# Performance work log

Hardware: AMD Instinct MI355X
Metric: run time of the kernel (lower is better)

Reference implementation:

```python
import jax, jax.numpy as jnp
import numpy as np

N_NODES = 50000
N_EDGES = 800000
N_GRAPHS = 2500
IN_DIM = 128
HID = 64
HEADS = 2
NEG_SLOPE = 0.2


def _gat_layer(x, W, att_src, att_dst, bias, src, dst, n):
    # W: [F_in, H*C], att_*: [H, C], bias: [C]
    h = (x @ W).reshape(n, HEADS, HID)            # [N,H,C]
    a_src = jnp.sum(h * att_src[None], axis=-1)   # [N,H]
    a_dst = jnp.sum(h * att_dst[None], axis=-1)   # [N,H]
    e = jax.nn.leaky_relu(a_src[src] + a_dst[dst], NEG_SLOPE)  # [E,H]
    # segment softmax over destination neighborhoods
    m = jax.ops.segment_max(e, dst, num_segments=n)            # [N,H]
    m = jnp.where(jnp.isfinite(m), m, 0.0)
    ex = jnp.exp(e - m[dst])
    s = jax.ops.segment_sum(ex, dst, num_segments=n)           # [N,H]
    alpha = ex / jnp.maximum(s[dst], 1e-16)                    # [E,H]
    msg = h[src] * alpha[:, :, None]                           # [E,H,C]
    out = jax.ops.segment_sum(msg, dst, num_segments=n)        # [N,H,C]
    return out.mean(axis=1) + bias                             # concat=False -> head mean


def _with_self_loops(edge_index, n):
    loop = jnp.arange(n, dtype=edge_index.dtype)
    src = jnp.concatenate([edge_index[0], loop])
    dst = jnp.concatenate([edge_index[1], loop])
    return src, dst


def setup_inputs() -> dict:
    key = jax.random.key(0)
    ks = jax.random.split(key, 16)
    x = jax.random.normal(ks[0], (N_NODES, IN_DIM), dtype=jnp.float32)
    edge_index = jax.random.randint(ks[1], (2, N_EDGES), 0, N_NODES, dtype=jnp.int32)
    batch = jnp.sort(jax.random.randint(ks[2], (N_NODES,), 0, N_GRAPHS, dtype=jnp.int32))

    def glorot(k, shape):
        fan = shape[0] + shape[-1]
        return jax.random.normal(k, shape, dtype=jnp.float32) * np.sqrt(2.0 / fan)

    inp = {"x": x, "edge_index": edge_index, "batch": batch}
    dims = [IN_DIM, HID, HID]
    for i in range(3):
        inp[f"W{i+1}"] = glorot(ks[3 + 4 * i], (dims[i], HEADS * HID))
        inp[f"att_src{i+1}"] = glorot(ks[4 + 4 * i], (HEADS, HID))
        inp[f"att_dst{i+1}"] = glorot(ks[5 + 4 * i], (HEADS, HID))
        inp[f"b{i+1}"] = jnp.zeros((HID,), dtype=jnp.float32)
    inp["lin_w"] = glorot(ks[15], (HID, 1))
    inp["lin_b"] = jnp.zeros((1,), dtype=jnp.float32)
    return inp


def reference(x, W1, att_src1, att_dst1, b1, W2, att_src2, att_dst2, b2,
              W3, att_src3, att_dst3, b3, lin_w, lin_b, edge_index, batch):
    n = x.shape[0]
    src, dst = _with_self_loops(edge_index, n)
    h = jax.nn.relu(_gat_layer(x, W1, att_src1, att_dst1, b1, src, dst, n))
    h = jax.nn.relu(_gat_layer(h, W2, att_src2, att_dst2, b2, src, dst, n))
    h = jax.nn.relu(_gat_layer(h, W3, att_src3, att_dst3, b3, src, dst, n))
    # global mean pool over graphs
    sums = jax.ops.segment_sum(h, batch, num_segments=N_GRAPHS)          # [G,C]
    cnt = jax.ops.segment_sum(jnp.ones((n,), h.dtype), batch, num_segments=N_GRAPHS)
    pooled = sums / jnp.maximum(cnt, 1.0)[:, None]
    return pooled @ lin_w + lin_b                                        # [G,1]
```

## Files before the change

### kernel.cpp

```cpp
#include <hip/hip_runtime.h>
#include <hip/hip_fp16.h>
#include <math.h>


__device__ __forceinline__ float lrelu(float v) { return v > 0.f ? v : 0.2f * v; }

__device__ __forceinline__ float wave_max(float v) {
  for (int off = 32; off; off >>= 1) v = fmaxf(v, __shfl_xor(v, off, 64));
  return v;
}
__device__ __forceinline__ float half_sum(float v) {
  for (int off = 16; off; off >>= 1) v += __shfl_xor(v, off, 64);
  return v;
}
__device__ __forceinline__ float half_max(float v) {
  for (int off = 16; off; off >>= 1) v = fmaxf(v, __shfl_xor(v, off, 64));
  return v;
}

__global__ void count_rank(const int* __restrict__ ei, int* __restrict__ deg,
                           int* __restrict__ rank, int e) {
  int j0 = blockIdx.x * 1024 + threadIdx.x;
#pragma unroll
  for (int k = 0; k < 4; ++k) {
    int j = j0 + k * 256;
    if (j < e) rank[j] = atomicAdd(&deg[ei[e + j]], 1);
  }
}

__global__ void scan_blocks(const int* __restrict__ deg, int* __restrict__ row_ptr,
                            int* __restrict__ btot, int n) {
  __shared__ int sm[256];
  int i = blockIdx.x * 256 + threadIdx.x;
  int v = (i < n) ? deg[i] : 0;
  sm[threadIdx.x] = v;
  __syncthreads();
  for (int off = 1; off < 256; off <<= 1) {
    int t = (threadIdx.x >= off) ? sm[threadIdx.x - off] : 0;
    __syncthreads();
    sm[threadIdx.x] += t;
    __syncthreads();
  }
  if (i < n) row_ptr[i] = sm[threadIdx.x] - v;
  if (threadIdx.x == 255) btot[blockIdx.x] = sm[255];
}

__global__ void scan_totals(int* __restrict__ btot, int nb) {
  __shared__ int sm[256];
  int v = (threadIdx.x < nb) ? btot[threadIdx.x] : 0;
  sm[threadIdx.x] = v;
  __syncthreads();
  for (int off = 1; off < 256; off <<= 1) {
    int t = (threadIdx.x >= off) ? sm[threadIdx.x - off] : 0;
    __syncthreads();
    sm[threadIdx.x] += t;
    __syncthreads();
  }
  if (threadIdx.x < nb) btot[threadIdx.x] = sm[threadIdx.x] - v;
}

__global__ void scan_add(int* __restrict__ row_ptr, int* __restrict__ csr,
                         const int* __restrict__ btot, int n, int total) {
  int i = blockIdx.x * 256 + threadIdx.x;
  if (i < n) {
    int v = row_ptr[i] + btot[blockIdx.x] + i;
    row_ptr[i] = v;
    csr[v] = i;
  }
  if (i == 0) row_ptr[n] = total;
}

__global__ void place_kernel(const int* __restrict__ ei, const int* __restrict__ rank,
                             const int* __restrict__ row_ptr, int* __restrict__ csr,
                             int e) {
  int j0 = blockIdx.x * 1024 + threadIdx.x;
#pragma unroll
  for (int k = 0; k < 4; ++k) {
    int j = j0 + k * 256;
    if (j < e) {
      int d = ei[e + j];
      csr[row_ptr[d] + 1 + rank[j]] = ei[j];
    }
  }
}

template <int K>
__global__ __launch_bounds__(256) void gemm_att(const float* __restrict__ X,
                                                const float* __restrict__ W,
                                                const float* __restrict__ asw,
                                                const float* __restrict__ adw,
                                                __half* __restrict__ H16,
                                                float* __restrict__ a_src,
                                                float* __restrict__ a_dst, int N) {
  __shared__ float Xs[64 * (K + 4)];
  int tid = threadIdx.x;
  int row0 = blockIdx.x * 64;
  int head = blockIdx.y;

  for (int idx = tid; idx < 64 * K; idx += 256) {
    int r = idx / K;
    int k = idx - r * K;
    int gr = row0 + r;
    if (gr >= N) gr = N - 1;
    Xs[r * (K + 4) + k] = X[(size_t)gr * K + k];
  }
  __syncthreads();

  int cgrp = tid & 15;
  int rg = tid >> 4;
  int c0 = head * 64 + cgrp * 4;
  const float* wp = W + c0;
  float acc[4][4] = {};

#pragma unroll 2
  for (int k = 0; k < K; k += 4) {
    float4 xr[4];
#pragma unroll
    for (int j = 0; j < 4; ++j)
      xr[j] = *(const float4*)(&Xs[(rg * 4 + j) * (K + 4) + k]);
#pragma unroll
    for (int kk = 0; kk < 4; ++kk) {
      float4 w4 = *(const float4*)(wp + (k + kk) * 128);
#pragma unroll
      for (int j = 0; j < 4; ++j) {
        float xv = ((const float*)&xr[j])[kk];
        acc[j][0] = fmaf(xv, w4.x, acc[j][0]);
        acc[j][1] = fmaf(xv, w4.y, acc[j][1]);
        acc[j][2] = fmaf(xv, w4.z, acc[j][2]);
        acc[j][3] = fmaf(xv, w4.w, acc[j][3]);
      }
    }
  }

  float4 aw = *(const float4*)(asw + c0);
  float4 dw = *(const float4*)(adw + c0);
#pragma unroll
  for (int j = 0; j < 4; ++j) {
    int r = row0 + rg * 4 + j;
    float sp = acc[j][0] * aw.x + acc[j][1] * aw.y + acc[j][2] * aw.z + acc[j][3] * aw.w;
    float dp = acc[j][0] * dw.x + acc[j][1] * dw.y + acc[j][2] * dw.z + acc[j][3] * dw.w;
#pragma unroll
    for (int off = 1; off < 16; off <<= 1) {
      sp += __shfl_xor(sp, off, 64);
      dp += __shfl_xor(dp, off, 64);
    }
    if (r < N) {
      union { __half2 h2[2]; uint2 u; } pk;
      pk.h2[0] = __floats2half2_rn(acc[j][0], acc[j][1]);
      pk.h2[1] = __floats2half2_rn(acc[j][2], acc[j][3]);
      *(uint2*)(H16 + (size_t)r * 128 + c0) = pk.u;
      if (cgrp == 0) {
        a_src[r * 2 + head] = sp;
        a_dst[r * 2 + head] = dp;
      }
    }
  }
}

__device__ __forceinline__ void ld_grp8(const __half* __restrict__ H16, int half_,
                                        int c8, int headsel, int sub, int s,
                                        float p0, float p1, int g,
                                        uint4* h, float* q) {
#pragma unroll
  for (int k = 0; k < 4; ++k) {
    int idx = half_ + g * 8 + k * 2 + sub;
    int st = __shfl(s, idx, 64);
    float q0 = __shfl(p0, idx, 64);
    float q1 = __shfl(p1, idx, 64);
    q[k] = headsel ? q1 : q0;
    h[k] = *(const uint4*)(H16 + (size_t)st * 128 + c8);
  }
}
__device__ __forceinline__ void fma_grp8(const uint4* h, const float* q,
                                         float* acc) {
#pragma unroll
  for (int k = 0; k < 4; ++k) {
    union { uint u; __half2 h2; } a, b, c, d;
    a.u = h[k].x; b.u = h[k].y; c.u = h[k].z; d.u = h[k].w;
    float2 f0 = __half22float2(a.h2);
    float2 f1 = __half22float2(b.h2);
    float2 f2 = __half22float2(c.h2);
    float2 f3 = __half22float2(d.h2);
    acc[0] = fmaf(f0.x, q[k], acc[0]);
    acc[1] = fmaf(f0.y, q[k], acc[1]);
    acc[2] = fmaf(f1.x, q[k], acc[2]);
    acc[3] = fmaf(f1.y, q[k], acc[3]);
    acc[4] = fmaf(f2.x, q[k], acc[4]);
    acc[5] = fmaf(f2.y, q[k], acc[5]);
    acc[6] = fmaf(f3.x, q[k], acc[6]);
    acc[7] = fmaf(f3.y, q[k], acc[7]);
  }
}
__device__ __forceinline__ void gather_pipe8(const __half* __restrict__ H16, int half_,
                                             int c8, int headsel, int sub, int s,
                                             float p0, float p1, int maxcnt,
                                             float* acc) {
  int groups = (maxcnt + 7) >> 3;
  uint4 ha[4], hb[4];
  float qa[4], qb[4];
  ld_grp8(H16, half_, c8, headsel, sub, s, p0, p1, 0, ha, qa);
  int g = 1;
  for (; g + 1 < groups; g += 2) {
    ld_grp8(H16, half_, c8, headsel, sub, s, p0, p1, g, hb, qb);
    fma_grp8(ha, qa, acc);
    ld_grp8(H16, half_, c8, headsel, sub, s, p0, p1, g + 1, ha, qa);
    fma_grp8(hb, qb, acc);
  }
  if (g < groups) {
    ld_grp8(H16, half_, c8, headsel, sub, s, p0, p1, g, hb, qb);
    fma_grp8(ha, qa, acc);
    fma_grp8(hb, qb, acc);
  } else {
    fma_grp8(ha, qa, acc);
  }
}

template <int POOL>
__global__ __launch_bounds__(256) void aggregate_fused(
    const __half* __restrict__ H16, const float* __restrict__ a_src,
    const float* __restrict__ a_dst, const float* __restrict__ bias,
    const int* __restrict__ row_ptr, const int* __restrict__ csr,
    float* __restrict__ out, const float* __restrict__ lw,
    float* __restrict__ pvn, int N) {
  int lane = threadIdx.x & 63;
  int half_ = lane & 32;
  int l32 = lane & 31;
  int dst = blockIdx.x * 8 + ((threadIdx.x >> 6) << 1) + (half_ >> 5);
  bool live = dst < N;
  int beg = live ? row_ptr[dst] : 0;
  int end = live ? row_ptr[dst + 1] : 0;
  int cnt = end - beg;
  float2 ad = live ? ((const float2*)a_dst)[dst] : make_float2(0.f, 0.f);
  int sub = l32 >> 4;
  int m = l32 & 15;
  int c8 = m * 8;
  int headsel = m >> 3;
  float acc[8] = {};
  float inv0, inv1;

  int maxcnt = (int)wave_max((float)cnt);
  if (maxcnt < 1) maxcnt = 1;

  if (maxcnt <= 32) {
    int j = beg + l32;
    bool valid = l32 < cnt;
    int s = valid ? csr[j] : 0;
    float2 as = ((const float2*)a_src)[s];
    float e0 = valid ? lrelu(as.x + ad.x) : -1e30f;
    float e1 = valid ? lrelu(as.y + ad.y) : -1e30f;
    float m0 = half_max(e0);
    float m1 = half_max(e1);
    float p0 = __expf(e0 - m0);
    float p1 = __expf(e1 - m1);
    inv0 = 1.f / fmaxf(half_sum(valid ? p0 : 0.f), 1e-16f);
    inv1 = 1.f / fmaxf(half_sum(valid ? p1 : 0.f), 1e-16f);
    gather_pipe8(H16, half_, c8, headsel, sub, s, p0, p1, maxcnt, acc);
  } else {
    float m0 = -1e30f, m1 = -1e30f, s0 = 0.f, s1 = 0.f;
    for (int base = 0; base < maxcnt; base += 32) {
      int j = beg + base + l32;
      bool valid = (base + l32) < cnt;
      int s = valid ? csr[j] : 0;
      float2 as = ((const float2*)a_src)[s];
      float e0 = valid ? lrelu(as.x + ad.x) : -1e30f;
      float e1 = valid ? lrelu(as.y + ad.y) : -1e30f;
      float nm0 = fmaxf(m0, half_max(e0));
      float nm1 = fmaxf(m1, half_max(e1));
      s0 = s0 * __expf(m0 - nm0) + half_sum(valid ? __expf(e0 - nm0) : 0.f);
      s1 = s1 * __expf(m1 - nm1) + half_sum(valid ? __expf(e1 - nm1) : 0.f);
      m0 = nm0; m1 = nm1;
    }
    inv0 = 1.f / fmaxf(s0, 1e-16f);
    inv1 = 1.f / fmaxf(s1, 1e-16f);
    for (int base = 0; base < maxcnt; base += 32) {
      int j = beg + base + l32;
      bool valid = (base + l32) < cnt;
      int s = valid ? csr[j] : 0;
      float2 as = ((const float2*)a_src)[s];
      float e0 = valid ? lrelu(as.x + ad.x) : -1e30f;
      float e1 = valid ? lrelu(as.y + ad.y) : -1e30f;
      float p0 = __expf(e0 - m0);
      float p1 = __expf(e1 - m1);
      int rem = maxcnt - base;
      if (rem > 32) rem = 32;
      gather_pipe8(H16, half_, c8, headsel, sub, s, p0, p1, rem, acc);
    }
  }

#pragma unroll
  for (int j = 0; j < 8; ++j) acc[j] += __shfl_xor(acc[j], 16, 64);

  float il = headsel ? inv1 : inv0;
  float v[8], w[8];
#pragma unroll
  for (int j = 0; j < 8; ++j) v[j] = acc[j] * il;
#pragma unroll
  for (int j = 0; j < 8; ++j) w[j] = __shfl_xor(v[j], 8, 64);

  if (m < 8 && sub == 0 && live) {
    int c = m * 8;
    float4 b0 = *(const float4*)(bias + c);
    float4 b1 = *(const float4*)(bias + c + 4);
    float r[8];
    r[0] = fmaxf(0.5f * (v[0] + w[0]) + b0.x, 0.f);
    r[1] = fmaxf(0.5f * (v[1] + w[1]) + b0.y, 0.f);
    r[2] = fmaxf(0.5f * (v[2] + w[2]) + b0.z, 0.f);
    r[3] = fmaxf(0.5f * (v[3] + w[3]) + b0.w, 0.f);
    r[4] = fmaxf(0.5f * (v[4] + w[4]) + b1.x, 0.f);
    r[5] = fmaxf(0.5f * (v[5] + w[5]) + b1.y, 0.f);
    r[6] = fmaxf(0.5f * (v[6] + w[6]) + b1.z, 0.f);
    r[7] = fmaxf(0.5f * (v[7] + w[7]) + b1.w, 0.f);
    if (POOL) {
      float4 l0 = *(const float4*)(lw + c);
      float4 l1 = *(const float4*)(lw + c + 4);
      float pv = r[0] * l0.x + r[1] * l0.y + r[2] * l0.z + r[3] * l0.w +
                 r[4] * l1.x + r[5] * l1.y + r[6] * l1.z + r[7] * l1.w;
      pv += __shfl_xor(pv, 1, 64);
      pv += __shfl_xor(pv, 2, 64);
      pv += __shfl_xor(pv, 4, 64);
      if (m == 0) pvn[dst] = pv;
    } else {
      *(float4*)(out + (size_t)dst * 64 + c) = make_float4(r[0], r[1], r[2], r[3]);
      *(float4*)(out + (size_t)dst * 64 + c + 4) = make_float4(r[4], r[5], r[6], r[7]);
    }
  }
}

__device__ __forceinline__ int lower_bound(const int* __restrict__ a, int n, int key) {
  int lo = 0, hi = n;
  while (lo < hi) {
    int mid = (lo + hi) >> 1;
    if (a[mid] < key) lo = mid + 1; else hi = mid;
  }
  return lo;
}

__global__ void finalize_kernel(const float* __restrict__ pvn,
                                const int* __restrict__ batch,
                                const float* __restrict__ lb,
                                float* __restrict__ out, int N, int G) {
  int g = blockIdx.x * blockDim.x + threadIdx.x;
  if (g >= G) return;
  int lo = lower_bound(batch, N, g);
  int hi = lower_bound(batch, N, g + 1);
  float s = 0.f;
  for (int i = lo; i < hi; ++i) s += pvn[i];
  out[g] = s / fmaxf((float)(hi - lo), 1.f) + lb[0];
}

extern "C" void kernel_launch(void* const* d_in, const int* in_sizes, int n_in,
                              void* d_out, int out_size, void* d_ws, size_t ws_size,
                              hipStream_t stream) {
  const float* x   = (const float*)d_in[0];
  const int* ei    = (const int*)d_in[1];
  const int* batch = (const int*)d_in[2];
  const float* W1  = (const float*)d_in[3];
  const float* as1 = (const float*)d_in[4];
  const float* ad1 = (const float*)d_in[5];
  const float* b1  = (const float*)d_in[6];
  const float* W2  = (const float*)d_in[7];
  const float* as2 = (const float*)d_in[8];
  const float* ad2 = (const float*)d_in[9];
  const float* b2  = (const float*)d_in[10];
  const float* W3  = (const float*)d_in[11];
  const float* as3 = (const float*)d_in[12];
  const float* ad3 = (const float*)d_in[13];
  const float* b3  = (const float*)d_in[14];
  const float* lw  = (const float*)d_in[15];
  const float* lb  = (const float*)d_in[16];
  float* out = (float*)d_out;

  const int N = in_sizes[0] / 128;
  const int E = in_sizes[1] / 2;
  const int ET = N + E;
  const int G = out_size;
  const int NB = (N + 255) / 256;

  char* p = (char*)d_ws;
  auto take = [&](size_t bytes) {
    char* r = p;
    p += (bytes + 255) & ~(size_t)255;
    return r;
  };
  int* deg      = (int*)take((size_t)N * 4);
  int* row_ptr  = (int*)take((size_t)(N + 1) * 4);
  int* rank     = (int*)take((size_t)E * 4);
  int* btot     = (int*)take((size_t)NB * 4);
  int* csr      = (int*)take((size_t)ET * 4);
  __half* H16   = (__half*)take((size_t)N * 128 * 2);
  float* a_src  = (float*)take((size_t)N * 2 * 4);
  float* a_dst  = (float*)take((size_t)N * 2 * 4);
  float* bufA   = (float*)take((size_t)N * 64 * 4);
  float* bufB   = (float*)take((size_t)N * 64 * 4);
  float* pvn    = (float*)take((size_t)N * 4);
  (void)ws_size; (void)n_in;

  hipMemsetAsync(deg, 0, (size_t)N * 4, stream);
  count_rank<<<(E + 1023) / 1024, 256, 0, stream>>>(ei, deg, rank, E);
  scan_blocks<<<NB, 256, 0, stream>>>(deg, row_ptr, btot, N);
  scan_totals<<<1, 256, 0, stream>>>(btot, NB);
  scan_add<<<NB, 256, 0, stream>>>(row_ptr, csr, btot, N, ET);
  place_kernel<<<(E + 1023) / 1024, 256, 0, stream>>>(ei, rank, row_ptr, csr, E);

  const dim3 gblk((N + 63) / 64, 2);
  const int ablk = (N + 7) / 8;

  gemm_att<128><<<gblk, 256, 0, stream>>>(x, W1, as1, ad1, H16, a_src, a_dst, N);
  aggregate_fused<0><<<ablk, 256, 0, stream>>>(H16, a_src, a_dst, b1, row_ptr, csr,
                                               bufA, lw, pvn, N);
  gemm_att<64><<<gblk, 256, 0, stream>>>(bufA, W2, as2, ad2, H16, a_src, a_dst, N);
  aggregate_fused<0><<<ablk, 256, 0, stream>>>(H16, a_src, a_dst, b2, row_ptr, csr,
                                               bufB, lw, pvn, N);
  gemm_att<64><<<gblk, 256, 0, stream>>>(bufB, W3, as3, ad3, H16, a_src, a_dst, N);
  aggregate_fused<1><<<ablk, 256, 0, stream>>>(H16, a_src, a_dst, b3, row_ptr, csr,
                                               bufA, lw, pvn, N);

  finalize_kernel<<<(G + 255) / 256, 256, 0, stream>>>(pvn, batch, lb, out, N, G);
}
```

Measured before the change: 347.8 us.

## Switch node projection GEMMs to fp16 MFMA with folded attention columns

Replaces the scalar FP32 GEMM with a matrix-core (MFMA 16x16x32 f16) kernel. Weights are pre-transposed and converted to fp16 in a prep step fused into the edge-count kernel, with the attention dot products folded in as extra output columns so a_src/a_dst come out of the same MFMA pass. Intermediate layer activations are stored as fp16 rather than fp32, halving their traffic, and the output columns are permuted to match the MFMA layout. Precision drops because inputs and activations are rounded to fp16 before each GEMM.

```diff
diff --git a/kernel.cpp b/kernel.cpp
--- a/kernel.cpp
+++ b/kernel.cpp
@@ -18,13 +18,60 @@
   return v;
 }
 
-__global__ void count_rank(const int* __restrict__ ei, int* __restrict__ deg,
-                           int* __restrict__ rank, int e) {
-  int j0 = blockIdx.x * 1024 + threadIdx.x;
-#pragma unroll
-  for (int k = 0; k < 4; ++k) {
-    int j = j0 + k * 256;
-    if (j < e) rank[j] = atomicAdd(&deg[ei[e + j]], 1);
+typedef _Float16 f16x8 __attribute__((ext_vector_type(8)));
+typedef float f32x4 __attribute__((ext_vector_type(4)));
+
+__device__ __forceinline__ int colperm(int l, int ks) {
+  return l == 0 ? ks : (((ks & 3) << 4) | ((ks >> 3) << 1) | ((ks >> 2) & 1));
+}
+
+__global__ void count_rank_prep(const int* __restrict__ ei, int* __restrict__ deg,
+                                int* __restrict__ rank, int e, int eb,
+                                const float* __restrict__ W1, const float* __restrict__ as1,
+                                const float* __restrict__ ad1,
+                                const float* __restrict__ W2, const float* __restrict__ as2,
+                                const float* __restrict__ ad2,
+                                const float* __restrict__ W3, const float* __restrict__ as3,
+                                const float* __restrict__ ad3,
+                                __half* __restrict__ WT1, __half* __restrict__ WT2,
+                                __half* __restrict__ WT3) {
+  int bx = blockIdx.x;
+  if (bx < eb) {
+    int j0 = bx * 1024 + threadIdx.x;
+#pragma unroll
+    for (int k = 0; k < 4; ++k) {
+      int j = j0 + k * 256;
+      if (j < e) rank[j] = atomicAdd(&deg[ei[e + j]], 1);
+    }
+    return;
+  }
+  int pb = bx - eb;
+  int l = pb >> 3, part = pb & 7;
+  const float* W = l == 0 ? W1 : (l == 1 ? W2 : W3);
+  const float* as = l == 0 ? as1 : (l == 1 ? as2 : as3);
+  const float* ad = l == 0 ? ad1 : (l == 1 ? ad2 : ad3);
+  __half* WT = l == 0 ? WT1 : (l == 1 ? WT2 : WT3);
+  const int shk = l == 0 ? 7 : 6;
+  const int K = 1 << shk;
+  for (int idx = part * 256 + threadIdx.x; idx < 144 * K; idx += 2048) {
+    int row = idx >> shk;
+    int ks = idx & (K - 1);
+    int kt = colperm(l, ks);
+    float val;
+    if (row < 128) {
+      val = W[kt * 128 + row];
+    } else if (row < 132) {
+      int j = row - 128;
+      const float* att = (j < 2 ? as : ad) + (j & 1) * 64;
+      const float* wr = W + kt * 128 + (j & 1) * 64;
+      float acc = 0.f;
+#pragma unroll
+      for (int c = 0; c < 64; ++c) acc = fmaf(wr[c], att[c], acc);
+      val = acc;
+    } else {
+      val = 0.f;
+    }
+    WT[idx] = __float2half(val);
   }
 }
 
@@ -84,75 +131,79 @@
   }
 }
 
-template <int K>
-__global__ __launch_bounds__(256) void gemm_att(const float* __restrict__ X,
-                                                const float* __restrict__ W,
-                                                const float* __restrict__ asw,
-                                                const float* __restrict__ adw,
-                                                __half* __restrict__ H16,
-                                                float* __restrict__ a_src,
-                                                float* __restrict__ a_dst, int N) {
-  __shared__ float Xs[64 * (K + 4)];
+template <int K, bool F16IN>
+__global__ __launch_bounds__(256) void gemm_mfma(const void* __restrict__ Xv,
+                                                 const __half* __restrict__ WT,
+                                                 __half* __restrict__ H16,
+                                                 float* __restrict__ a_src,
+                                                 float* __restrict__ a_dst, int N) {
+  constexpr int KP = K + 8;
+  extern __shared__ __half smem[];
+  __half* Al = smem;
+  __half* Wl = smem + 64 * KP;
   int tid = threadIdx.x;
   int row0 = blockIdx.x * 64;
-  int head = blockIdx.y;
-
-  for (int idx = tid; idx < 64 * K; idx += 256) {
-    int r = idx / K;
-    int k = idx - r * K;
-    int gr = row0 + r;
-    if (gr >= N) gr = N - 1;
-    Xs[r * (K + 4) + k] = X[(size_t)gr * K + k];
+
+  if constexpr (F16IN) {
+    const __half* X = (const __half*)Xv;
+    constexpr int CH = K / 8;
+    for (int idx = tid; idx < 64 * CH; idx += 256) {
+      int r = idx / CH, ch = idx % CH;
+      int gr = row0 + r; if (gr >= N) gr = N - 1;
+      *(uint4*)&Al[r * KP + ch * 8] = *(const uint4*)(X + (size_t)gr * K + ch * 8);
+    }
+  } else {
+    const float* X = (const float*)Xv;
+    constexpr int CH4 = K / 4;
+    for (int idx = tid; idx < 64 * CH4; idx += 256) {
+      int r = idx / CH4, ch = idx % CH4;
+      int gr = row0 + r; if (gr >= N) gr = N - 1;
+      float4 v = *(const float4*)(X + (size_t)gr * K + ch * 4);
+      union { __half2 h2[2]; uint2 u; } t;
+      t.h2[0] = __floats2half2_rn(v.x, v.y);
+      t.h2[1] = __floats2half2_rn(v.z, v.w);
+      *(uint2*)&Al[r * KP + ch * 4] = t.u;
+    }
+  }
+  constexpr int CHW = K / 8;
+  for (int idx = tid; idx < 144 * CHW; idx += 256) {
+    int r = idx / CHW, ch = idx % CHW;
+    *(uint4*)&Wl[r * KP + ch * 8] = *(const uint4*)(WT + r * K + ch * 8);
   }
   __syncthreads();
 
-  int cgrp = tid & 15;
-  int rg = tid >> 4;
-  int c0 = head * 64 + cgrp * 4;
-  const float* wp = W + c0;
-  float acc[4][4] = {};
-
-#pragma unroll 2
-  for (int k = 0; k < K; k += 4) {
-    float4 xr[4];
-#pragma unroll
-    for (int j = 0; j < 4; ++j)
-      xr[j] = *(const float4*)(&Xs[(rg * 4 + j) * (K + 4) + k]);
-#pragma unroll
-    for (int kk = 0; kk < 4; ++kk) {
-      float4 w4 = *(const float4*)(wp + (k + kk) * 128);
-#pragma unroll
-      for (int j = 0; j < 4; ++j) {
-        float xv = ((const float*)&xr[j])[kk];
-        acc[j][0] = fmaf(xv, w4.x, acc[j][0]);
-        acc[j][1] = fmaf(xv, w4.y, acc[j][1]);
-        acc[j][2] = fmaf(xv, w4.z, acc[j][2]);
-        acc[j][3] = fmaf(xv, w4.w, acc[j][3]);
-      }
-    }
-  }
-
-  float4 aw = *(const float4*)(asw + c0);
-  float4 dw = *(const float4*)(adw + c0);
-#pragma unroll
-  for (int j = 0; j < 4; ++j) {
-    int r = row0 + rg * 4 + j;
-    float sp = acc[j][0] * aw.x + acc[j][1] * aw.y + acc[j][2] * aw.z + acc[j][3] * aw.w;
-    float dp = acc[j][0] * dw.x + acc[j][1] * dw.y + acc[j][2] * dw.z + acc[j][3] * dw.w;
-#pragma unroll
-    for (int off = 1; off < 16; off <<= 1) {
-      sp += __shfl_xor(sp, off, 64);
-      dp += __shfl_xor(dp, off, 64);
-    }
+  int lane = tid & 63;
+  int wv = tid >> 6;
+  int q = lane & 15;
+  int kg = lane >> 4;
+
+  f32x4 acc[9] = {};
+  const __half* ap = &Al[(wv * 16 + q) * KP + kg * 8];
+  const __half* wp = &Wl[q * KP + kg * 8];
+#pragma unroll
+  for (int ks = 0; ks < K / 32; ++ks) {
+    f16x8 a = *(const f16x8*)(ap + ks * 32);
+#pragma unroll
+    for (int n = 0; n < 9; ++n) {
+      f16x8 b = *(const f16x8*)(wp + n * 16 * KP + ks * 32);
+      acc[n] = __builtin_amdgcn_mfma_f32_16x16x32_f16(a, b, acc[n], 0, 0, 0);
+    }
+  }
+
+#pragma unroll
+  for (int reg = 0; reg < 4; ++reg) {
+    int r = row0 + wv * 16 + kg * 4 + reg;
     if (r < N) {
-      union { __half2 h2[2]; uint2 u; } pk;
-      pk.h2[0] = __floats2half2_rn(acc[j][0], acc[j][1]);
-      pk.h2[1] = __floats2half2_rn(acc[j][2], acc[j][3]);
-      *(uint2*)(H16 + (size_t)r * 128 + c0) = pk.u;
-      if (cgrp == 0) {
-        a_src[r * 2 + head] = sp;
-        a_dst[r * 2 + head] = dp;
-      }
+      union { __half2 h2[2]; uint2 u; } s0, s1;
+      s0.h2[0] = __floats2half2_rn(acc[0][reg], acc[1][reg]);
+      s0.h2[1] = __floats2half2_rn(acc[2][reg], acc[3][reg]);
+      s1.h2[0] = __floats2half2_rn(acc[4][reg], acc[5][reg]);
+      s1.h2[1] = __floats2half2_rn(acc[6][reg], acc[7][reg]);
+      *(uint2*)(H16 + (size_t)r * 128 + q * 4) = s0.u;
+      *(uint2*)(H16 + (size_t)r * 128 + 64 + q * 4) = s1.u;
+      float av = acc[8][reg];
+      if (q < 2) a_src[r * 2 + q] = av;
+      else if (q < 4) a_dst[r * 2 + q - 2] = av;
     }
   }
 }
@@ -220,7 +271,7 @@
     const __half* __restrict__ H16, const float* __restrict__ a_src,
     const float* __restrict__ a_dst, const float* __restrict__ bias,
     const int* __restrict__ row_ptr, const int* __restrict__ csr,
-    float* __restrict__ out, const float* __restrict__ lw,
+    __half* __restrict__ out, const float* __restrict__ lw,
     float* __restrict__ pvn, int N) {
   int lane = threadIdx.x & 63;
   int half_ = lane & 32;
@@ -298,30 +349,31 @@
   for (int j = 0; j < 8; ++j) w[j] = __shfl_xor(v[j], 8, 64);
 
   if (m < 8 && sub == 0 && live) {
-    int c = m * 8;
-    float4 b0 = *(const float4*)(bias + c);
-    float4 b1 = *(const float4*)(bias + c + 4);
+    int cb = m << 1;
     float r[8];
-    r[0] = fmaxf(0.5f * (v[0] + w[0]) + b0.x, 0.f);
-    r[1] = fmaxf(0.5f * (v[1] + w[1]) + b0.y, 0.f);
-    r[2] = fmaxf(0.5f * (v[2] + w[2]) + b0.z, 0.f);
-    r[3] = fmaxf(0.5f * (v[3] + w[3]) + b0.w, 0.f);
-    r[4] = fmaxf(0.5f * (v[4] + w[4]) + b1.x, 0.f);
-    r[5] = fmaxf(0.5f * (v[5] + w[5]) + b1.y, 0.f);
-    r[6] = fmaxf(0.5f * (v[6] + w[6]) + b1.z, 0.f);
-    r[7] = fmaxf(0.5f * (v[7] + w[7]) + b1.w, 0.f);
+#pragma unroll
+    for (int j = 0; j < 8; ++j) {
+      int c = ((j & 3) << 4) + cb + (j >> 2);
+      r[j] = fmaxf(0.5f * (v[j] + w[j]) + bias[c], 0.f);
+    }
     if (POOL) {
-      float4 l0 = *(const float4*)(lw + c);
-      float4 l1 = *(const float4*)(lw + c + 4);
-      float pv = r[0] * l0.x + r[1] * l0.y + r[2] * l0.z + r[3] * l0.w +
-                 r[4] * l1.x + r[5] * l1.y + r[6] * l1.z + r[7] * l1.w;
+      float pv = 0.f;
+#pragma unroll
+      for (int j = 0; j < 8; ++j) {
+        int c = ((j & 3) << 4) + cb + (j >> 2);
+        pv = fmaf(r[j], lw[c], pv);
+      }
       pv += __shfl_xor(pv, 1, 64);
       pv += __shfl_xor(pv, 2, 64);
       pv += __shfl_xor(pv, 4, 64);
       if (m == 0) pvn[dst] = pv;
     } else {
-      *(float4*)(out + (size_t)dst * 64 + c) = make_float4(r[0], r[1], r[2], r[3]);
-      *(float4*)(out + (size_t)dst * 64 + c + 4) = make_float4(r[4], r[5], r[6], r[7]);
+      union { __half2 h2[4]; uint4 u; } pk;
+      pk.h2[0] = __floats2half2_rn(r[0], r[1]);
+      pk.h2[1] = __floats2half2_rn(r[2], r[3]);
+      pk.h2[2] = __floats2half2_rn(r[4], r[5]);
+      pk.h2[3] = __floats2half2_rn(r[6], r[7]);
+      *(uint4*)(out + (size_t)dst * 64 + m * 8) = pk.u;
     }
   }
 }
@@ -375,6 +427,7 @@
   const int ET = N + E;
   const int G = out_size;
   const int NB = (N + 255) / 256;
+  const int EB = (E + 1023) / 1024;
 
   char* p = (char*)d_ws;
   auto take = [&](size_t bytes) {
@@ -390,28 +443,35 @@
   __half* H16   = (__half*)take((size_t)N * 128 * 2);
   float* a_src  = (float*)take((size_t)N * 2 * 4);
   float* a_dst  = (float*)take((size_t)N * 2 * 4);
-  float* bufA   = (float*)take((size_t)N * 64 * 4);
-  float* bufB   = (float*)take((size_t)N * 64 * 4);
+  __half* bufA  = (__half*)take((size_t)N * 64 * 2);
+  __half* bufB  = (__half*)take((size_t)N * 64 * 2);
   float* pvn    = (float*)take((size_t)N * 4);
+  __half* WT1   = (__half*)take((size_t)144 * 128 * 2);
+  __half* WT2   = (__half*)take((size_t)144 * 64 * 2);
+  __half* WT3   = (__half*)take((size_t)144 * 64 * 2);
   (void)ws_size; (void)n_in;
 
   hipMemsetAsync(deg, 0, (size_t)N * 4, stream);
-  count_rank<<<(E + 1023) / 1024, 256, 0, stream>>>(ei, deg, rank, E);
+  count_rank_prep<<<EB + 24, 256, 0, stream>>>(ei, deg, rank, E, EB,
+                                               W1, as1, ad1, W2, as2, ad2,
+                                               W3, as3, ad3, WT1, WT2, WT3);
   scan_blocks<<<NB, 256, 0, stream>>>(deg, row_ptr, btot, N);
   scan_totals<<<1, 256, 0, stream>>>(btot, NB);
   scan_add<<<NB, 256, 0, stream>>>(row_ptr, csr, btot, N, ET);
-  place_kernel<<<(E + 1023) / 1024, 256, 0, stream>>>(ei, rank, row_ptr, csr, E);
-
-  const dim3 gblk((N + 63) / 64, 2);
+  place_kernel<<<EB, 256, 0, stream>>>(ei, rank, row_ptr, csr, E);
+
+  const int gblk = (N + 63) / 64;
   const int ablk = (N + 7) / 8;
-
-  gemm_att<128><<<gblk, 256, 0, stream>>>(x, W1, as1, ad1, H16, a_src, a_dst, N);
+  constexpr int LDS1 = (64 + 144) * (128 + 8) * 2;
+  constexpr int LDS2 = (64 + 144) * (64 + 8) * 2;
+
+  gemm_mfma<128, false><<<gblk, 256, LDS1, stream>>>(x, WT1, H16, a_src, a_dst, N);
   aggregate_fused<0><<<ablk, 256, 0, stream>>>(H16, a_src, a_dst, b1, row_ptr, csr,
                                                bufA, lw, pvn, N);
-  gemm_att<64><<<gblk, 256, 0, stream>>>(bufA, W2, as2, ad2, H16, a_src, a_dst, N);
+  gemm_mfma<64, true><<<gblk, 256, LDS2, stream>>>(bufA, WT2, H16, a_src, a_dst, N);
   aggregate_fused<0><<<ablk, 256, 0, stream>>>(H16, a_src, a_dst, b2, row_ptr, csr,
                                                bufB, lw, pvn, N);
-  gemm_att<64><<<gblk, 256, 0, stream>>>(bufB, W3, as3, ad3, H16, a_src, a_dst, N);
+  gemm_mfma<64, true><<<gblk, 256, LDS2, stream>>>(bufB, WT3, H16, a_src, a_dst, N);
   aggregate_fused<1><<<ablk, 256, 0, stream>>>(H16, a_src, a_dst, b3, row_ptr, csr,
                                                bufA, lw, pvn, N);
 
```

Result: faster. 308.8 us (-11.2%).
